# Kernel tuning notes

Hardware: AMD Instinct MI355X
Metric: run time of the kernel (lower is better)

The kernel has to match this reference:

```python
import jax, jax.numpy as jnp
import numpy as np


def setup_inputs() -> dict:
    key = jax.random.key(0)
    k1, k2 = jax.random.split(key)
    NUM_INS, NUM_CLASS = 8192, 5000
    # probabilities strictly inside (0,1) so log terms are finite
    output = jax.random.uniform(k1, (NUM_INS, NUM_CLASS), dtype=jnp.float32,
                                minval=1e-6, maxval=1.0 - 1e-6)
    # labels in {0,1,2}; 2 == ignore
    target = jax.random.randint(k2, (NUM_INS, NUM_CLASS), 0, 3, dtype=jnp.int64)
    return {"output": output, "target": target}


def reference(output, target):
    is_pos = target == 1
    is_neg = target == 0
    # masked BCE: -log(p) for positives, -log(1-p) for negatives, 0 where target==2
    per_elem = jnp.where(is_pos, -jnp.log(output),
                         jnp.where(is_neg, -jnp.log1p(-output), 0.0))
    count = jnp.sum(is_pos | is_neg)
    cost = jnp.sum(per_elem) / count.astype(per_elem.dtype)
    return cost
```

## Files before the change

kernel.cpp:

```cpp
#include <hip/hip_runtime.h>


#define GRID_BLOCKS 1000
#define BLOCK 256
#define UNROLL 8

__global__ __launch_bounds__(BLOCK) void bce_reduce_kernel(
    const float* __restrict__ prob,
    const int* __restrict__ tgt,
    float* __restrict__ part_sum,
    unsigned int* __restrict__ part_cnt,
    int n)
{
    const int tid    = blockIdx.x * BLOCK + threadIdx.x;
    const int stride = GRID_BLOCKS * BLOCK;
    const int n4     = n >> 2;

    float        lsum = 0.0f;
    unsigned int lcnt = 0u;

    const float4* __restrict__ p4 = (const float4*)prob;
    const int4*   __restrict__ t4 = (const int4*)tgt;

    #define ACC(P, T)                                   \
    {                                                   \
        float v = ((T) == 1) ? (P) : 1.0f - (P);        \
        bool  c = (unsigned)(T) <= 1u;                  \
        float l = -__logf(v);                           \
        lsum += c ? l : 0.0f;                           \
        lcnt += c ? 1u : 0u;                            \
    }
    #define ACC4(P, T) ACC((P).x,(T).x) ACC((P).y,(T).y) ACC((P).z,(T).z) ACC((P).w,(T).w)

    int i = tid;
    for (; i + (UNROLL - 1) * stride < n4; i += UNROLL * stride) {
        float4 p[UNROLL];
        int4   t[UNROLL];
        #pragma unroll
        for (int j = 0; j < UNROLL; ++j) {
            p[j] = p4[i + j * stride];
            t[j] = t4[i + j * stride];
        }
        #pragma unroll
        for (int j = 0; j < UNROLL; ++j) {
            ACC4(p[j], t[j])
        }
    }
    for (; i < n4; i += stride) {
        float4 p = p4[i];
        int4   t = t4[i];
        ACC4(p, t)
    }
    for (int k = (n4 << 2) + tid; k < n; k += stride) {
        float p = prob[k];
        int   t = tgt[k];
        ACC(p, t)
    }

    #pragma unroll
    for (int off = 32; off > 0; off >>= 1) {
        lsum += __shfl_down(lsum, off, 64);
        lcnt += __shfl_down(lcnt, off, 64);
    }

    __shared__ float        s_sum[4];
    __shared__ unsigned int s_cnt[4];
    const int lane = threadIdx.x & 63;
    const int wave = threadIdx.x >> 6;
    if (lane == 0) { s_sum[wave] = lsum; s_cnt[wave] = lcnt; }
    __syncthreads();
    if (threadIdx.x == 0) {
        part_sum[blockIdx.x] = s_sum[0] + s_sum[1] + s_sum[2] + s_sum[3];
        part_cnt[blockIdx.x] = s_cnt[0] + s_cnt[1] + s_cnt[2] + s_cnt[3];
    }
}

__global__ __launch_bounds__(BLOCK) void bce_finalize_kernel(
    const float* __restrict__ part_sum,
    const unsigned int* __restrict__ part_cnt,
    float* __restrict__ out)
{
    float        lsum = 0.0f;
    unsigned int lcnt = 0u;
    for (int i = threadIdx.x; i < GRID_BLOCKS; i += BLOCK) {
        lsum += part_sum[i];
        lcnt += part_cnt[i];
    }
    #pragma unroll
    for (int off = 32; off > 0; off >>= 1) {
        lsum += __shfl_down(lsum, off, 64);
        lcnt += __shfl_down(lcnt, off, 64);
    }
    __shared__ float        s_sum[4];
    __shared__ unsigned int s_cnt[4];
    const int lane = threadIdx.x & 63;
    const int wave = threadIdx.x >> 6;
    if (lane == 0) { s_sum[wave] = lsum; s_cnt[wave] = lcnt; }
    __syncthreads();
    if (threadIdx.x == 0) {
        float        bsum = s_sum[0] + s_sum[1] + s_sum[2] + s_sum[3];
        unsigned int bcnt = s_cnt[0] + s_cnt[1] + s_cnt[2] + s_cnt[3];
        out[0] = bsum / (float)bcnt;
    }
}

extern "C" void kernel_launch(void* const* d_in, const int* in_sizes, int n_in,
                              void* d_out, int out_size, void* d_ws, size_t ws_size,
                              hipStream_t stream) {
    const float* prob = (const float*)d_in[0];
    const int*   tgt  = (const int*)d_in[1];
    float*       out  = (float*)d_out;

    const int n = in_sizes[0];

    float*        part_sum = (float*)d_ws;
    unsigned int* part_cnt = (unsigned int*)((char*)d_ws + GRID_BLOCKS * sizeof(float));

    bce_reduce_kernel<<<GRID_BLOCKS, BLOCK, 0, stream>>>(prob, tgt, part_sum, part_cnt, n);
    bce_finalize_kernel<<<1, BLOCK, 0, stream>>>(part_sum, part_cnt, out);
}
```

Measured before the change: 330.5 us.

## Stage loads via global_load_lds double buffering per wave

Replaces the register-unrolled float4 streaming loop with per-wave async global-to-LDS loads (global_load_lds, 16 bytes per lane) into a double buffer. The next chunk is prefetched while the current one is consumed, using manual vmcnt waits. The grid also grows from 1000 to 2048 blocks. The aim is to keep more memory traffic in flight without register pressure, at the cost of an extra LDS round trip and only one chunk of lookahead per wave, which may expose less memory-level parallelism than the 8-way unroll it replaces.

```diff
diff --git a/kernel.cpp b/kernel.cpp
--- a/kernel.cpp
+++ b/kernel.cpp
@@ -1,26 +1,35 @@
 #include <hip/hip_runtime.h>
+#include <stdint.h>
 
 
-#define GRID_BLOCKS 1000
+#define GRID_BLOCKS 2048
 #define BLOCK 256
-#define UNROLL 8
+#define WAVES_PER_BLOCK 4
+#define CHUNK_ELEMS 256
+
+#define WAITCNT_VM(N) (((N) & 0xF) | (0x7 << 4) | (0xF << 8) | ((((N) >> 4) & 0x3) << 14))
+
+typedef __attribute__((address_space(3))) void       lds_void_t;
+typedef const __attribute__((address_space(1))) void gbl_void_t;
 
 __global__ __launch_bounds__(BLOCK) void bce_reduce_kernel(
     const float* __restrict__ prob,
     const int* __restrict__ tgt,
     float* __restrict__ part_sum,
     unsigned int* __restrict__ part_cnt,
+    int nchunk,
     int n)
 {
-    const int tid    = blockIdx.x * BLOCK + threadIdx.x;
-    const int stride = GRID_BLOCKS * BLOCK;
-    const int n4     = n >> 2;
+    __shared__ float lds_p[WAVES_PER_BLOCK][2][CHUNK_ELEMS];
+    __shared__ int   lds_t[WAVES_PER_BLOCK][2][CHUNK_ELEMS];
+
+    const int lane = threadIdx.x & 63;
+    const int wave = threadIdx.x >> 6;
+    const int wgid = blockIdx.x * WAVES_PER_BLOCK + wave;
+    const int W    = GRID_BLOCKS * WAVES_PER_BLOCK;
 
     float        lsum = 0.0f;
     unsigned int lcnt = 0u;
-
-    const float4* __restrict__ p4 = (const float4*)prob;
-    const int4*   __restrict__ t4 = (const int4*)tgt;
 
     #define ACC(P, T)                                   \
     {                                                   \
@@ -32,29 +41,43 @@
     }
     #define ACC4(P, T) ACC((P).x,(T).x) ACC((P).y,(T).y) ACC((P).z,(T).z) ACC((P).w,(T).w)
 
-    int i = tid;
-    for (; i + (UNROLL - 1) * stride < n4; i += UNROLL * stride) {
-        float4 p[UNROLL];
-        int4   t[UNROLL];
-        #pragma unroll
-        for (int j = 0; j < UNROLL; ++j) {
-            p[j] = p4[i + j * stride];
-            t[j] = t4[i + j * stride];
+    #define STAGE(c, b)                                                        \
+    {                                                                          \
+        __builtin_amdgcn_global_load_lds(                                      \
+            (gbl_void_t*)(prob + (size_t)(c) * CHUNK_ELEMS + lane * 4),        \
+            (lds_void_t*)&lds_p[wave][(b)][0], 16, 0, 0);                      \
+        __builtin_amdgcn_global_load_lds(                                      \
+            (gbl_void_t*)(tgt  + (size_t)(c) * CHUNK_ELEMS + lane * 4),        \
+            (lds_void_t*)&lds_t[wave][(b)][0], 16, 0, 0);                      \
+    }
+
+    int c   = wgid;
+    int buf = 0;
+    if (c < nchunk) {
+        STAGE(c, 0)
+    }
+    while (c < nchunk) {
+        const int cn = c + W;
+        if (cn < nchunk) {
+            STAGE(cn, buf ^ 1)
+            __builtin_amdgcn_s_waitcnt(WAITCNT_VM(2));
+        } else {
+            __builtin_amdgcn_s_waitcnt(WAITCNT_VM(0));
         }
-        #pragma unroll
-        for (int j = 0; j < UNROLL; ++j) {
-            ACC4(p[j], t[j])
+        const float4 p = *(const float4*)&lds_p[wave][buf][lane * 4];
+        const int4   t = *(const int4*)&lds_t[wave][buf][lane * 4];
+        ACC4(p, t)
+        buf ^= 1;
+        c = cn;
+    }
+
+    {
+        const int gtid = blockIdx.x * BLOCK + threadIdx.x;
+        for (int k = nchunk * CHUNK_ELEMS + gtid; k < n; k += GRID_BLOCKS * BLOCK) {
+            float p = prob[k];
+            int   t = tgt[k];
+            ACC(p, t)
         }
-    }
-    for (; i < n4; i += stride) {
-        float4 p = p4[i];
-        int4   t = t4[i];
-        ACC4(p, t)
-    }
-    for (int k = (n4 << 2) + tid; k < n; k += stride) {
-        float p = prob[k];
-        int   t = tgt[k];
-        ACC(p, t)
     }
 
     #pragma unroll
@@ -63,10 +86,8 @@
         lcnt += __shfl_down(lcnt, off, 64);
     }
 
-    __shared__ float        s_sum[4];
-    __shared__ unsigned int s_cnt[4];
-    const int lane = threadIdx.x & 63;
-    const int wave = threadIdx.x >> 6;
+    __shared__ float        s_sum[WAVES_PER_BLOCK];
+    __shared__ unsigned int s_cnt[WAVES_PER_BLOCK];
     if (lane == 0) { s_sum[wave] = lsum; s_cnt[wave] = lcnt; }
     __syncthreads();
     if (threadIdx.x == 0) {
@@ -111,11 +132,12 @@
     const int*   tgt  = (const int*)d_in[1];
     float*       out  = (float*)d_out;
 
-    const int n = in_sizes[0];
+    const int n      = in_sizes[0];
+    const int nchunk = n / CHUNK_ELEMS;
 
     float*        part_sum = (float*)d_ws;
     unsigned int* part_cnt = (unsigned int*)((char*)d_ws + GRID_BLOCKS * sizeof(float));
 
-    bce_reduce_kernel<<<GRID_BLOCKS, BLOCK, 0, stream>>>(prob, tgt, part_sum, part_cnt, n);
+    bce_reduce_kernel<<<GRID_BLOCKS, BLOCK, 0, stream>>>(prob, tgt, part_sum, part_cnt, nchunk, n);
     bce_finalize_kernel<<<1, BLOCK, 0, stream>>>(part_sum, part_cnt, out);
 }
```

After: 330.4 us. About the same (-0.0%).
